# Performance work log

Hardware: AMD Instinct MI355X
Metric: run time of the kernel (lower is better)

The kernel has to match this reference:

```python
import jax, jax.numpy as jnp
import numpy as np

# Per-layer (in_dim, hidden) for the 6 stacked LSTM layers:
# rnn_inp: (1,64),(64,64),(64,64); rnn_out: (64,1),(1,1),(1,1)
_LAYER_DIMS = [(1, 64), (64, 64), (64, 64), (64, 1), (1, 1), (1, 1)]
_LAYER_NAMES = ['a0', 'a1', 'a2', 'b0', 'b1', 'b2']


def _lstm_layer(x, w_ih, w_hh, b_ih, b_hh):
    """Single unidirectional LSTM layer, PyTorch gate order (i, f, g, o).
    x: [B, T, Din]; w_ih: [4H, Din]; w_hh: [4H, H]; biases: [4H]. Returns [B, T, H]."""
    H = w_hh.shape[1]
    B = x.shape[0]
    # Input projection for all timesteps at once (one big GEMM).
    pre = jnp.einsum('btd,gd->btg', x, w_ih) + b_ih + b_hh  # [B, T, 4H]
    pre_t = jnp.swapaxes(pre, 0, 1)  # [T, B, 4H]

    def step(carry, xt):
        h, c = carry
        gates = xt + h @ w_hh.T  # [B, 4H]
        i, f, g, o = jnp.split(gates, 4, axis=-1)
        i = jax.nn.sigmoid(i)
        f = jax.nn.sigmoid(f)
        g = jnp.tanh(g)
        o = jax.nn.sigmoid(o)
        c = f * c + i * g
        h = o * jnp.tanh(c)
        return (h, c), h

    h0 = jnp.zeros((B, H), x.dtype)
    (_, _), hs = jax.lax.scan(step, (h0, h0), pre_t)  # hs: [T, B, H]
    return jnp.swapaxes(hs, 0, 1)


def setup_inputs() -> dict:
    key = jax.random.key(0)
    B, T = 256, 512
    inp = {}
    k, key = jax.random.split(key)
    inp['x'] = jax.random.normal(k, (B, T, 1), dtype=jnp.float32)
    for name, (din, h) in zip(_LAYER_NAMES, _LAYER_DIMS):
        s = 1.0 / np.sqrt(h)  # PyTorch LSTM init scale U(-1/sqrt(H), 1/sqrt(H))
        k1, k2, k3, k4, key = jax.random.split(key, 5)
        inp[f'w_ih_{name}'] = jax.random.uniform(k1, (4 * h, din), jnp.float32, -s, s)
        inp[f'w_hh_{name}'] = jax.random.uniform(k2, (4 * h, h), jnp.float32, -s, s)
        inp[f'b_ih_{name}'] = jax.random.uniform(k3, (4 * h,), jnp.float32, -s, s)
        inp[f'b_hh_{name}'] = jax.random.uniform(k4, (4 * h,), jnp.float32, -s, s)
    return inp


def reference(x,
              w_ih_a0, w_hh_a0, b_ih_a0, b_hh_a0,
              w_ih_a1, w_hh_a1, b_ih_a1, b_hh_a1,
              w_ih_a2, w_hh_a2, b_ih_a2, b_hh_a2,
              w_ih_b0, w_hh_b0, b_ih_b0, b_hh_b0,
              w_ih_b1, w_hh_b1, b_ih_b1, b_hh_b1,
              w_ih_b2, w_hh_b2, b_ih_b2, b_hh_b2):
    layers = [
        (w_ih_a0, w_hh_a0, b_ih_a0, b_hh_a0),
        (w_ih_a1, w_hh_a1, b_ih_a1, b_hh_a1),
        (w_ih_a2, w_hh_a2, b_ih_a2, b_hh_a2),
        (w_ih_b0, w_hh_b0, b_ih_b0, b_hh_b0),
        (w_ih_b1, w_hh_b1, b_ih_b1, b_hh_b1),
        (w_ih_b2, w_hh_b2, b_ih_b2, b_hh_b2),
    ]
    h = x
    for w_ih, w_hh, b_ih, b_hh in layers:
        h = _lstm_layer(h, w_ih, w_hh, b_ih, b_hh)
    # activation between the two LSTM stacks is identity (activation_type='identity')
    return h  # [B, T, 1]
```

## Files before the change

kernel.cpp:

```cpp
#include <hip/hip_runtime.h>


#define BB 256
#define TT 512
#define CH 4
#define NS 8

typedef _Float16 v2h __attribute__((ext_vector_type(2)));

__device__ __forceinline__ float sig_(float x) {
  return __builtin_amdgcn_rcpf(1.f + __builtin_amdgcn_exp2f(-1.44269504f * x));
}
__device__ __forceinline__ float tanh_(float x) {
  return __builtin_fmaf(2.f, __builtin_amdgcn_rcpf(1.f + __builtin_amdgcn_exp2f(-2.88539008f * x)), -1.f);
}

template <int K>
__device__ __forceinline__ float qb_(float v) {
  return __int_as_float(__builtin_amdgcn_update_dpp(
      0, __float_as_int(v), (K | (K << 2) | (K << 4) | (K << 6)), 0xF, 0xF, true));
}

__device__ __forceinline__ void ldsbar_() {
  asm volatile("s_waitcnt lgkmcnt(0)\n\ts_barrier" ::: "memory");
}

#if __has_builtin(__builtin_amdgcn_fdot2)
#define FDOT2(acc, a, b) (acc) = __builtin_amdgcn_fdot2((a), (b), (acc), false)
#else
#define FDOT2(acc, a, b) \
  (acc) = __builtin_fmaf((float)(a)[0], (float)(b)[0], \
          __builtin_fmaf((float)(a)[1], (float)(b)[1], (acc)))
#endif
#define KEEPP(a) asm volatile("" : "+v"(a))
#define PIN32(w)                                                            \
  do {                                                                      \
    _Pragma("unroll") for (int _i = 0; _i < 32; ++_i) KEEPP((w)[_i]);       \
  } while (0)

__device__ __forceinline__ v2h bc2h_(int v) { return __builtin_bit_cast(v2h, v); }

__device__ __forceinline__ void load_h64(const _Float16* p, v2h hv[32]) {
  const int4* hp = reinterpret_cast<const int4*>(p);
#pragma unroll
  for (int i = 0; i < 8; ++i) {
    int4 blk = hp[i];
    hv[4 * i + 0] = bc2h_(blk.x);
    hv[4 * i + 1] = bc2h_(blk.y);
    hv[4 * i + 2] = bc2h_(blk.z);
    hv[4 * i + 3] = bc2h_(blk.w);
  }
}

__device__ __forceinline__ void load_row16(const float* src, v2h dst[32]) {
  const float4* p = reinterpret_cast<const float4*>(src);
#pragma unroll
  for (int i = 0; i < 16; ++i) {
    float4 v = p[i];
    dst[2 * i]     = v2h{(_Float16)v.x, (_Float16)v.y};
    dst[2 * i + 1] = v2h{(_Float16)v.z, (_Float16)v.w};
  }
}

__device__ __forceinline__ void dot4_(const v2h w[4][32], const v2h hv[32],
                                      float& p0, float& p1, float& p2, float& p3) {
  float a0 = p0, a1 = p1, a2 = p2, a3 = p3;
  float b0 = 0.f, b1 = 0.f, b2 = 0.f, b3 = 0.f;
#pragma unroll
  for (int j = 0; j < 32; j += 2) {
    FDOT2(a0, w[0][j], hv[j]);         FDOT2(a1, w[1][j], hv[j]);
    FDOT2(a2, w[2][j], hv[j]);         FDOT2(a3, w[3][j], hv[j]);
    FDOT2(b0, w[0][j + 1], hv[j + 1]); FDOT2(b1, w[1][j + 1], hv[j + 1]);
    FDOT2(b2, w[2][j + 1], hv[j + 1]); FDOT2(b3, w[3][j + 1], hv[j + 1]);
  }
  p0 = a0 + b0; p1 = a1 + b1; p2 = a2 + b2; p3 = a3 + b3;
}

__device__ __forceinline__ void dot2g_(const v2h* w0, const v2h* w1,
                                       const v2h hv[32], float& p0, float& p1) {
  float a0 = 0.f, a1 = 0.f, b0 = 0.f, b1 = 0.f;
#pragma unroll
  for (int j = 0; j < 32; j += 2) {
    FDOT2(a0, w0[j], hv[j]);         FDOT2(a1, w1[j], hv[j]);
    FDOT2(b0, w0[j + 1], hv[j + 1]); FDOT2(b1, w1[j + 1], hv[j + 1]);
  }
  p0 = a0 + b0; p1 = a1 + b1;
}

__global__ __attribute__((amdgpu_flat_work_group_size(512, 512),
                          amdgpu_waves_per_eu(1, 2)))
void lstm_pipe_k(
    const float* __restrict__ x,
    const float* __restrict__ wih_a0, const float* __restrict__ whh_a0,
    const float* __restrict__ bih_a0, const float* __restrict__ bhh_a0,
    const float* __restrict__ wih_a1, const float* __restrict__ whh_a1,
    const float* __restrict__ bih_a1, const float* __restrict__ bhh_a1,
    const float* __restrict__ wih_a2, const float* __restrict__ whh_a2,
    const float* __restrict__ bih_a2, const float* __restrict__ bhh_a2,
    const float* __restrict__ wih_b0, const float* __restrict__ whh_b0,
    const float* __restrict__ bih_b0, const float* __restrict__ bhh_b0,
    const float* __restrict__ wih_b1, const float* __restrict__ whh_b1,
    const float* __restrict__ bih_b1, const float* __restrict__ bhh_b1,
    const float* __restrict__ wih_b2, const float* __restrict__ whh_b2,
    const float* __restrict__ bih_b2, const float* __restrict__ bhh_b2,
    float* __restrict__ out)
{
  asm volatile("" ::: "v190", "v191");

  const int b = blockIdx.x;
  const int tid = threadIdx.x;
  const int wave = tid >> 6;
  const int lane = tid & 63;

  __shared__ __align__(16) _Float16 hh[3][NS][64];
  __shared__ __align__(16) float pj[2][NS][256];
  __shared__ float xs[TT];

  for (int i = tid; i < TT; i += 512) xs[i] = x[(size_t)b * TT + i];
  for (int i = tid; i < 3 * NS * 64 / 2; i += 512) reinterpret_cast<int*>(hh)[i] = 0;

  v2h wt[4][32];
  float bias[4] = {0.f, 0.f, 0.f, 0.f};
  float wi0_[4] = {0.f, 0.f, 0.f, 0.f};
  float whb0[4] = {}, wi1b[4] = {}, wh1b[4] = {}, bb1[4] = {},
        wi2b[4] = {}, wh2b[4] = {}, bb2[4] = {};

  if (wave == 0) {
#pragma unroll
    for (int q = 0; q < 4; ++q) {
      const int row = q * 64 + lane;
      load_row16(whh_a0 + row * 64, wt[q]);
      bias[q] = bih_a0[row] + bhh_a0[row];
      wi0_[q] = wih_a0[row];
    }
    PIN32(wt[0]); PIN32(wt[1]); PIN32(wt[2]); PIN32(wt[3]);
  } else if (wave == 1) {
#pragma unroll
    for (int q = 0; q < 4; ++q) {
      const int row = q * 64 + lane;
      load_row16(whh_a1 + row * 64, wt[q]);
      bias[q] = bih_a1[row] + bhh_a1[row];
    }
    PIN32(wt[0]); PIN32(wt[1]); PIN32(wt[2]); PIN32(wt[3]);
  } else if (wave == 2) {
#pragma unroll
    for (int q = 0; q < 4; ++q) {
      const int row = q * 64 + lane;
      load_row16(whh_a2 + row * 64, wt[q]);
      bias[q] = bih_a2[row] + bhh_a2[row];
    }
    PIN32(wt[0]); PIN32(wt[1]); PIN32(wt[2]); PIN32(wt[3]);
  } else if (wave == 3) {
    const int q = lane & 3;
    load_row16(wih_b0 + q * 64, wt[0]);
    bias[0] = bih_b0[q] + bhh_b0[q];
#pragma unroll
    for (int k = 0; k < 4; ++k) {
      whb0[k] = whh_b0[k];
      wi1b[k] = wih_b1[k]; wh1b[k] = whh_b1[k]; bb1[k] = bih_b1[k] + bhh_b1[k];
      wi2b[k] = wih_b2[k]; wh2b[k] = whh_b2[k]; bb2[k] = bih_b2[k] + bhh_b2[k];
    }
    PIN32(wt[0]);
  } else if (wave == 4) {
#pragma unroll
    for (int q = 0; q < 2; ++q) load_row16(wih_a1 + (q * 64 + lane) * 64, wt[q]);
    PIN32(wt[0]); PIN32(wt[1]);
  } else if (wave == 5) {
#pragma unroll
    for (int q = 0; q < 2; ++q) load_row16(wih_a1 + ((q + 2) * 64 + lane) * 64, wt[q]);
    PIN32(wt[0]); PIN32(wt[1]);
  } else if (wave == 6) {
#pragma unroll
    for (int q = 0; q < 2; ++q) load_row16(wih_a2 + (q * 64 + lane) * 64, wt[q]);
    PIN32(wt[0]); PIN32(wt[1]);
  } else {
#pragma unroll
    for (int q = 0; q < 2; ++q) load_row16(wih_a2 + ((q + 2) * 64 + lane) * 64, wt[q]);
    PIN32(wt[0]); PIN32(wt[1]);
  }
  __syncthreads();

  float c = 0.f;
  float h0b = 0.f, c0b = 0.f, h1b = 0.f, c1b = 0.f, h2b = 0.f, c2b = 0.f;

  const int NE = TT / CH + 5;
  for (int e = 0; e < NE; ++e) {
    if (wave == 0) {
      const int t0 = e * CH;
      if (t0 < TT) {
        __builtin_amdgcn_s_setprio(1);
        for (int s = 0; s < CH; ++s) {
          const int t = t0 + s;
          v2h hv[32];
          load_h64(&hh[0][(t + NS - 1) & (NS - 1)][0], hv);
          const float xv = xs[t];
          float p0 = bias[0], p1 = bias[1], p2 = bias[2], p3 = bias[3];
          dot4_(wt, hv, p0, p1, p2, p3);
          p0 = __builtin_fmaf(wi0_[0], xv, p0);
          p1 = __builtin_fmaf(wi0_[1], xv, p1);
          p2 = __builtin_fmaf(wi0_[2], xv, p2);
          p3 = __builtin_fmaf(wi0_[3], xv, p3);
          float gi = sig_(p0), gf = sig_(p1), gg = tanh_(p2), go = sig_(p3);
          c = __builtin_fmaf(gf, c, gi * gg);
          hh[0][t & (NS - 1)][lane] = (_Float16)(go * tanh_(c));
          asm volatile("s_waitcnt lgkmcnt(0)" ::: "memory");
        }
        __builtin_amdgcn_s_setprio(0);
      }
    } else if (wave == 1) {
      const int t0 = (e - 2) * CH;
      if (t0 >= 0 && t0 < TT) {
        __builtin_amdgcn_s_setprio(1);
        for (int s = 0; s < CH; ++s) {
          const int t = t0 + s;
          v2h hv[32];
          load_h64(&hh[1][(t + NS - 1) & (NS - 1)][0], hv);
          float4 pr = *reinterpret_cast<const float4*>(&pj[0][t & (NS - 1)][lane * 4]);
          float p0 = bias[0], p1 = bias[1], p2 = bias[2], p3 = bias[3];
          dot4_(wt, hv, p0, p1, p2, p3);
          p0 += pr.x; p1 += pr.y; p2 += pr.z; p3 += pr.w;
          float gi = sig_(p0), gf = sig_(p1), gg = tanh_(p2), go = sig_(p3);
          c = __builtin_fmaf(gf, c, gi * gg);
          hh[1][t & (NS - 1)][lane] = (_Float16)(go * tanh_(c));
          asm volatile("s_waitcnt lgkmcnt(0)" ::: "memory");
        }
        __builtin_amdgcn_s_setprio(0);
      }
    } else if (wave == 2) {
      const int t0 = (e - 4) * CH;
      if (t0 >= 0 && t0 < TT) {
        __builtin_amdgcn_s_setprio(1);
        for (int s = 0; s < CH; ++s) {
          const int t = t0 + s;
          v2h hv[32];
          load_h64(&hh[2][(t + NS - 1) & (NS - 1)][0], hv);
          float4 pr = *reinterpret_cast<const float4*>(&pj[1][t & (NS - 1)][lane * 4]);
          float p0 = bias[0], p1 = bias[1], p2 = bias[2], p3 = bias[3];
          dot4_(wt, hv, p0, p1, p2, p3);
          p0 += pr.x; p1 += pr.y; p2 += pr.z; p3 += pr.w;
          float gi = sig_(p0), gf = sig_(p1), gg = tanh_(p2), go = sig_(p3);
          c = __builtin_fmaf(gf, c, gi * gg);
          hh[2][t & (NS - 1)][lane] = (_Float16)(go * tanh_(c));
          asm volatile("s_waitcnt lgkmcnt(0)" ::: "memory");
        }
        __builtin_amdgcn_s_setprio(0);
      }
    } else if (wave == 3) {
      const int t0 = (e - 5) * CH;
      if (t0 >= 0 && t0 < TT) {
        for (int s = 0; s < CH; ++s) {
          const int t = t0 + s;
          v2h hv[32];
          load_h64(&hh[2][t & (NS - 1)][0], hv);
          float pga = bias[0], pgb = 0.f;
#pragma unroll
          for (int j = 0; j < 32; j += 2) {
            FDOT2(pga, wt[0][j], hv[j]);
            FDOT2(pgb, wt[0][j + 1], hv[j + 1]);
          }
          float pg = pga + pgb;
          float p_i = qb_<0>(pg), p_f = qb_<1>(pg), p_g = qb_<2>(pg), p_o = qb_<3>(pg);
          float i0 = sig_(__builtin_fmaf(whb0[0], h0b, p_i));
          float f0 = sig_(__builtin_fmaf(whb0[1], h0b, p_f));
          float g0 = tanh_(__builtin_fmaf(whb0[2], h0b, p_g));
          float o0 = sig_(__builtin_fmaf(whb0[3], h0b, p_o));
          c0b = __builtin_fmaf(f0, c0b, i0 * g0);
          h0b = o0 * tanh_(c0b);
          float i1 = sig_(bb1[0] + __builtin_fmaf(wi1b[0], h0b, wh1b[0] * h1b));
          float f1 = sig_(bb1[1] + __builtin_fmaf(wi1b[1], h0b, wh1b[1] * h1b));
          float g1 = tanh_(bb1[2] + __builtin_fmaf(wi1b[2], h0b, wh1b[2] * h1b));
          float o1 = sig_(bb1[3] + __builtin_fmaf(wi1b[3], h0b, wh1b[3] * h1b));
          c1b = __builtin_fmaf(f1, c1b, i1 * g1);
          h1b = o1 * tanh_(c1b);
          float i2 = sig_(bb2[0] + __builtin_fmaf(wi2b[0], h1b, wh2b[0] * h2b));
          float f2 = sig_(bb2[1] + __builtin_fmaf(wi2b[1], h1b, wh2b[1] * h2b));
          float g2 = tanh_(bb2[2] + __builtin_fmaf(wi2b[2], h1b, wh2b[2] * h2b));
          float o2 = sig_(bb2[3] + __builtin_fmaf(wi2b[3], h1b, wh2b[3] * h2b));
          c2b = __builtin_fmaf(f2, c2b, i2 * g2);
          h2b = o2 * tanh_(c2b);
          if (lane == 0) out[(size_t)b * TT + t] = h2b;
        }
      }
    } else if (wave == 4) {
      const int t0 = (e - 1) * CH;
      if (t0 >= 0 && t0 < TT) {
        for (int s = 0; s < CH; ++s) {
          const int t = t0 + s;
          v2h hv[32];
          load_h64(&hh[0][t & (NS - 1)][0], hv);
          float p0, p1;
          dot2g_(wt[0], wt[1], hv, p0, p1);
          *reinterpret_cast<float2*>(&pj[0][t & (NS - 1)][lane * 4]) = float2{p0, p1};
        }
      }
    } else if (wave == 5) {
      const int t0 = (e - 1) * CH;
      if (t0 >= 0 && t0 < TT) {
        for (int s = 0; s < CH; ++s) {
          const int t = t0 + s;
          v2h hv[32];
          load_h64(&hh[0][t & (NS - 1)][0], hv);
          float p2, p3;
          dot2g_(wt[0], wt[1], hv, p2, p3);
          *reinterpret_cast<float2*>(&pj[0][t & (NS - 1)][lane * 4 + 2]) = float2{p2, p3};
        }
      }
    } else if (wave == 6) {
      const int t0 = (e - 3) * CH;
      if (t0 >= 0 && t0 < TT) {
        for (int s = 0; s < CH; ++s) {
          const int t = t0 + s;
          v2h hv[32];
          load_h64(&hh[1][t & (NS - 1)][0], hv);
          float p0, p1;
          dot2g_(wt[0], wt[1], hv, p0, p1);
          *reinterpret_cast<float2*>(&pj[1][t & (NS - 1)][lane * 4]) = float2{p0, p1};
        }
      }
    } else {
      const int t0 = (e - 3) * CH;
      if (t0 >= 0 && t0 < TT) {
        for (int s = 0; s < CH; ++s) {
          const int t = t0 + s;
          v2h hv[32];
          load_h64(&hh[1][t & (NS - 1)][0], hv);
          float p2, p3;
          dot2g_(wt[0], wt[1], hv, p2, p3);
          *reinterpret_cast<float2*>(&pj[1][t & (NS - 1)][lane * 4 + 2]) = float2{p2, p3};
        }
      }
    }
    ldsbar_();
  }
}

extern "C" void kernel_launch(void* const* d_in, const int* in_sizes, int n_in,
                              void* d_out, int out_size, void* d_ws, size_t ws_size,
                              hipStream_t stream) {
  const float* x      = (const float*)d_in[0];
  const float* wih_a0 = (const float*)d_in[1];
  const float* whh_a0 = (const float*)d_in[2];
  const float* bih_a0 = (const float*)d_in[3];
  const float* bhh_a0 = (const float*)d_in[4];
  const float* wih_a1 = (const float*)d_in[5];
  const float* whh_a1 = (const float*)d_in[6];
  const float* bih_a1 = (const float*)d_in[7];
  const float* bhh_a1 = (const float*)d_in[8];
  const float* wih_a2 = (const float*)d_in[9];
  const float* whh_a2 = (const float*)d_in[10];
  const float* bih_a2 = (const float*)d_in[11];
  const float* bhh_a2 = (const float*)d_in[12];
  const float* wih_b0 = (const float*)d_in[13];
  const float* whh_b0 = (const float*)d_in[14];
  const float* bih_b0 = (const float*)d_in[15];
  const float* bhh_b0 = (const float*)d_in[16];
  const float* wih_b1 = (const float*)d_in[17];
  const float* whh_b1 = (const float*)d_in[18];
  const float* bih_b1 = (const float*)d_in[19];
  const float* bhh_b1 = (const float*)d_in[20];
  const float* wih_b2 = (const float*)d_in[21];
  const float* whh_b2 = (const float*)d_in[22];
  const float* bih_b2 = (const float*)d_in[23];
  const float* bhh_b2 = (const float*)d_in[24];
  float* out = (float*)d_out;

  lstm_pipe_k<<<BB, 512, 0, stream>>>(
      x,
      wih_a0, whh_a0, bih_a0, bhh_a0,
      wih_a1, whh_a1, bih_a1, bhh_a1,
      wih_a2, whh_a2, bih_a2, bhh_a2,
      wih_b0, whh_b0, bih_b0, bhh_b0,
      wih_b1, whh_b1, bih_b1, bhh_b1,
      wih_b2, whh_b2, bih_b2, bhh_b2,
      out);
}
```

Before: 401.5 us.

## Spill half of recurrent weights to LDS to fit two blocks per CU

Each recurrent wave now keeps only the first 32 columns of its 256x64 W_hh slice in registers and stages the rest as packed fp16 rows in LDS. Each step reads those rows back with int4 loads. This halves weight register pressure, so waves_per_eu can rise to 2 and two 512-thread blocks can share a CU. It also doubles the pipeline chunk (CH 8, NS 16) to halve barrier count, and drops the per-step lgkmcnt waits after the h stores. The cost is extra LDS traffic on the serial recurrence critical path and more shared memory per block. Removing the explicit waits may weaken ordering of the h writes within a chunk.

```diff
diff --git a/kernel.cpp b/kernel.cpp
--- a/kernel.cpp
+++ b/kernel.cpp
@@ -3,8 +3,8 @@
 
 #define BB 256
 #define TT 512
-#define CH 4
-#define NS 8
+#define CH 8
+#define NS 16
 
 typedef _Float16 v2h __attribute__((ext_vector_type(2)));
 
@@ -33,12 +33,15 @@
           __builtin_fmaf((float)(a)[1], (float)(b)[1], (acc)))
 #endif
 #define KEEPP(a) asm volatile("" : "+v"(a))
-#define PIN32(w)                                                            \
+#define PIN16(w)                                                            \
   do {                                                                      \
-    _Pragma("unroll") for (int _i = 0; _i < 32; ++_i) KEEPP((w)[_i]);       \
+    _Pragma("unroll") for (int _i = 0; _i < 16; ++_i) KEEPP((w)[_i]);       \
   } while (0)
 
 __device__ __forceinline__ v2h bc2h_(int v) { return __builtin_bit_cast(v2h, v); }
+__device__ __forceinline__ int pk2_(float x, float y) {
+  return __builtin_bit_cast(int, v2h{(_Float16)x, (_Float16)y});
+}
 
 __device__ __forceinline__ void load_h64(const _Float16* p, v2h hv[32]) {
   const int4* hp = reinterpret_cast<const int4*>(p);
@@ -52,43 +55,95 @@
   }
 }
 
-__device__ __forceinline__ void load_row16(const float* src, v2h dst[32]) {
+__device__ __forceinline__ void load_row_pair(const float* src, v2h lo[16], v2h hi[16]) {
   const float4* p = reinterpret_cast<const float4*>(src);
 #pragma unroll
-  for (int i = 0; i < 16; ++i) {
+  for (int i = 0; i < 8; ++i) {
     float4 v = p[i];
-    dst[2 * i]     = v2h{(_Float16)v.x, (_Float16)v.y};
-    dst[2 * i + 1] = v2h{(_Float16)v.z, (_Float16)v.w};
-  }
-}
-
-__device__ __forceinline__ void dot4_(const v2h w[4][32], const v2h hv[32],
-                                      float& p0, float& p1, float& p2, float& p3) {
+    lo[2 * i]     = v2h{(_Float16)v.x, (_Float16)v.y};
+    lo[2 * i + 1] = v2h{(_Float16)v.z, (_Float16)v.w};
+  }
+#pragma unroll
+  for (int i = 0; i < 8; ++i) {
+    float4 v = p[8 + i];
+    hi[2 * i]     = v2h{(_Float16)v.x, (_Float16)v.y};
+    hi[2 * i + 1] = v2h{(_Float16)v.z, (_Float16)v.w};
+  }
+}
+
+__device__ __forceinline__ void load_rec_w(const float* W, int lane,
+                                           v2h wt[4][16], unsigned char* wl) {
+#pragma unroll
+  for (int q = 0; q < 4; ++q) {
+    const int row = q * 64 + lane;
+    const float4* p = reinterpret_cast<const float4*>(W + row * 64);
+#pragma unroll
+    for (int i = 0; i < 8; ++i) {
+      float4 v = p[i];
+      wt[q][2 * i]     = v2h{(_Float16)v.x, (_Float16)v.y};
+      wt[q][2 * i + 1] = v2h{(_Float16)v.z, (_Float16)v.w};
+    }
+#pragma unroll
+    for (int i = 0; i < 4; ++i) {
+      float4 va = p[8 + 2 * i], vb = p[9 + 2 * i];
+      int4 blk;
+      blk.x = pk2_(va.x, va.y); blk.y = pk2_(va.z, va.w);
+      blk.z = pk2_(vb.x, vb.y); blk.w = pk2_(vb.z, vb.w);
+      *reinterpret_cast<int4*>(wl + row * 80 + i * 16) = blk;
+    }
+  }
+}
+
+__device__ __forceinline__ void dot4full_(const v2h wt[4][16],
+                                          const unsigned char* wl, int lane,
+                                          const v2h hv[32],
+                                          float& p0, float& p1, float& p2, float& p3) {
   float a0 = p0, a1 = p1, a2 = p2, a3 = p3;
   float b0 = 0.f, b1 = 0.f, b2 = 0.f, b3 = 0.f;
 #pragma unroll
-  for (int j = 0; j < 32; j += 2) {
-    FDOT2(a0, w[0][j], hv[j]);         FDOT2(a1, w[1][j], hv[j]);
-    FDOT2(a2, w[2][j], hv[j]);         FDOT2(a3, w[3][j], hv[j]);
-    FDOT2(b0, w[0][j + 1], hv[j + 1]); FDOT2(b1, w[1][j + 1], hv[j + 1]);
-    FDOT2(b2, w[2][j + 1], hv[j + 1]); FDOT2(b3, w[3][j + 1], hv[j + 1]);
+  for (int j = 0; j < 16; j += 2) {
+    FDOT2(a0, wt[0][j], hv[j]);         FDOT2(a1, wt[1][j], hv[j]);
+    FDOT2(a2, wt[2][j], hv[j]);         FDOT2(a3, wt[3][j], hv[j]);
+    FDOT2(b0, wt[0][j + 1], hv[j + 1]); FDOT2(b1, wt[1][j + 1], hv[j + 1]);
+    FDOT2(b2, wt[2][j + 1], hv[j + 1]); FDOT2(b3, wt[3][j + 1], hv[j + 1]);
+  }
+  const int rb0 = lane * 80, rb1 = (64 + lane) * 80,
+            rb2 = (128 + lane) * 80, rb3 = (192 + lane) * 80;
+#pragma unroll
+  for (int jb = 0; jb < 4; ++jb) {
+    int4 w0 = *reinterpret_cast<const int4*>(wl + rb0 + jb * 16);
+    int4 w1 = *reinterpret_cast<const int4*>(wl + rb1 + jb * 16);
+    int4 w2 = *reinterpret_cast<const int4*>(wl + rb2 + jb * 16);
+    int4 w3 = *reinterpret_cast<const int4*>(wl + rb3 + jb * 16);
+    const int h0 = 16 + jb * 4;
+    FDOT2(a0, bc2h_(w0.x), hv[h0 + 0]); FDOT2(b0, bc2h_(w0.y), hv[h0 + 1]);
+    FDOT2(a0, bc2h_(w0.z), hv[h0 + 2]); FDOT2(b0, bc2h_(w0.w), hv[h0 + 3]);
+    FDOT2(a1, bc2h_(w1.x), hv[h0 + 0]); FDOT2(b1, bc2h_(w1.y), hv[h0 + 1]);
+    FDOT2(a1, bc2h_(w1.z), hv[h0 + 2]); FDOT2(b1, bc2h_(w1.w), hv[h0 + 3]);
+    FDOT2(a2, bc2h_(w2.x), hv[h0 + 0]); FDOT2(b2, bc2h_(w2.y), hv[h0 + 1]);
+    FDOT2(a2, bc2h_(w2.z), hv[h0 + 2]); FDOT2(b2, bc2h_(w2.w), hv[h0 + 3]);
+    FDOT2(a3, bc2h_(w3.x), hv[h0 + 0]); FDOT2(b3, bc2h_(w3.y), hv[h0 + 1]);
+    FDOT2(a3, bc2h_(w3.z), hv[h0 + 2]); FDOT2(b3, bc2h_(w3.w), hv[h0 + 3]);
   }
   p0 = a0 + b0; p1 = a1 + b1; p2 = a2 + b2; p3 = a3 + b3;
 }
 
-__device__ __forceinline__ void dot2g_(const v2h* w0, const v2h* w1,
+__device__ __forceinline__ void dot2g_(const v2h* wa_lo, const v2h* wa_hi,
+                                       const v2h* wb_lo, const v2h* wb_hi,
                                        const v2h hv[32], float& p0, float& p1) {
   float a0 = 0.f, a1 = 0.f, b0 = 0.f, b1 = 0.f;
 #pragma unroll
-  for (int j = 0; j < 32; j += 2) {
-    FDOT2(a0, w0[j], hv[j]);         FDOT2(a1, w1[j], hv[j]);
-    FDOT2(b0, w0[j + 1], hv[j + 1]); FDOT2(b1, w1[j + 1], hv[j + 1]);
+  for (int j = 0; j < 16; j += 2) {
+    FDOT2(a0, wa_lo[j], hv[j]);          FDOT2(b0, wa_lo[j + 1], hv[j + 1]);
+    FDOT2(a0, wa_hi[j], hv[16 + j]);     FDOT2(b0, wa_hi[j + 1], hv[17 + j]);
+    FDOT2(a1, wb_lo[j], hv[j]);          FDOT2(b1, wb_lo[j + 1], hv[j + 1]);
+    FDOT2(a1, wb_hi[j], hv[16 + j]);     FDOT2(b1, wb_hi[j + 1], hv[17 + j]);
   }
   p0 = a0 + b0; p1 = a1 + b1;
 }
 
 __global__ __attribute__((amdgpu_flat_work_group_size(512, 512),
-                          amdgpu_waves_per_eu(1, 2)))
+                          amdgpu_waves_per_eu(2, 2)))
 void lstm_pipe_k(
     const float* __restrict__ x,
     const float* __restrict__ wih_a0, const float* __restrict__ whh_a0,
@@ -105,8 +160,6 @@
     const float* __restrict__ bih_b2, const float* __restrict__ bhh_b2,
     float* __restrict__ out)
 {
-  asm volatile("" ::: "v190", "v191");
-
   const int b = blockIdx.x;
   const int tid = threadIdx.x;
   const int wave = tid >> 6;
@@ -114,45 +167,46 @@
 
   __shared__ __align__(16) _Float16 hh[3][NS][64];
   __shared__ __align__(16) float pj[2][NS][256];
+  __shared__ __align__(16) unsigned char wlds[3][256 * 80];
   __shared__ float xs[TT];
 
   for (int i = tid; i < TT; i += 512) xs[i] = x[(size_t)b * TT + i];
   for (int i = tid; i < 3 * NS * 64 / 2; i += 512) reinterpret_cast<int*>(hh)[i] = 0;
 
-  v2h wt[4][32];
+  v2h wt[4][16];
   float bias[4] = {0.f, 0.f, 0.f, 0.f};
   float wi0_[4] = {0.f, 0.f, 0.f, 0.f};
   float whb0[4] = {}, wi1b[4] = {}, wh1b[4] = {}, bb1[4] = {},
         wi2b[4] = {}, wh2b[4] = {}, bb2[4] = {};
 
   if (wave == 0) {
+    load_rec_w(whh_a0, lane, wt, &wlds[0][0]);
 #pragma unroll
     for (int q = 0; q < 4; ++q) {
       const int row = q * 64 + lane;
-      load_row16(whh_a0 + row * 64, wt[q]);
       bias[q] = bih_a0[row] + bhh_a0[row];
       wi0_[q] = wih_a0[row];
     }
-    PIN32(wt[0]); PIN32(wt[1]); PIN32(wt[2]); PIN32(wt[3]);
+    PIN16(wt[0]); PIN16(wt[1]); PIN16(wt[2]); PIN16(wt[3]);
   } else if (wave == 1) {
+    load_rec_w(whh_a1, lane, wt, &wlds[1][0]);
 #pragma unroll
     for (int q = 0; q < 4; ++q) {
       const int row = q * 64 + lane;
-      load_row16(whh_a1 + row * 64, wt[q]);
       bias[q] = bih_a1[row] + bhh_a1[row];
     }
-    PIN32(wt[0]); PIN32(wt[1]); PIN32(wt[2]); PIN32(wt[3]);
+    PIN16(wt[0]); PIN16(wt[1]); PIN16(wt[2]); PIN16(wt[3]);
   } else if (wave == 2) {
+    load_rec_w(whh_a2, lane, wt, &wlds[2][0]);
 #pragma unroll
     for (int q = 0; q < 4; ++q) {
       const int row = q * 64 + lane;
-      load_row16(whh_a2 + row * 64, wt[q]);
       bias[q] = bih_a2[row] + bhh_a2[row];
     }
-    PIN32(wt[0]); PIN32(wt[1]); PIN32(wt[2]); PIN32(wt[3]);
+    PIN16(wt[0]); PIN16(wt[1]); PIN16(wt[2]); PIN16(wt[3]);
   } else if (wave == 3) {
     const int q = lane & 3;
-    load_row16(wih_b0 + q * 64, wt[0]);
+    load_row_pair(wih_b0 + q * 64, wt[0], wt[1]);
     bias[0] = bih_b0[q] + bhh_b0[q];
 #pragma unroll
     for (int k = 0; k < 4; ++k) {
@@ -160,23 +214,23 @@
       wi1b[k] = wih_b1[k]; wh1b[k] = whh_b1[k]; bb1[k] = bih_b1[k] + bhh_b1[k];
       wi2b[k] = wih_b2[k]; wh2b[k] = whh_b2[k]; bb2[k] = bih_b2[k] + bhh_b2[k];
     }
-    PIN32(wt[0]);
+    PIN16(wt[0]); PIN16(wt[1]);
   } else if (wave == 4) {
-#pragma unroll
-    for (int q = 0; q < 2; ++q) load_row16(wih_a1 + (q * 64 + lane) * 64, wt[q]);
-    PIN32(wt[0]); PIN32(wt[1]);
+    load_row_pair(wih_a1 + (0 * 64 + lane) * 64, wt[0], wt[1]);
+    load_row_pair(wih_a1 + (1 * 64 + lane) * 64, wt[2], wt[3]);
+    PIN16(wt[0]); PIN16(wt[1]); PIN16(wt[2]); PIN16(wt[3]);
   } else if (wave == 5) {
-#pragma unroll
-    for (int q = 0; q < 2; ++q) load_row16(wih_a1 + ((q + 2) * 64 + lane) * 64, wt[q]);
-    PIN32(wt[0]); PIN32(wt[1]);
+    load_row_pair(wih_a1 + (2 * 64 + lane) * 64, wt[0], wt[1]);
+    load_row_pair(wih_a1 + (3 * 64 + lane) * 64, wt[2], wt[3]);
+    PIN16(wt[0]); PIN16(wt[1]); PIN16(wt[2]); PIN16(wt[3]);
   } else if (wave == 6) {
-#pragma unroll
-    for (int q = 0; q < 2; ++q) load_row16(wih_a2 + (q * 64 + lane) * 64, wt[q]);
-    PIN32(wt[0]); PIN32(wt[1]);
+    load_row_pair(wih_a2 + (0 * 64 + lane) * 64, wt[0], wt[1]);
+    load_row_pair(wih_a2 + (1 * 64 + lane) * 64, wt[2], wt[3]);
+    PIN16(wt[0]); PIN16(wt[1]); PIN16(wt[2]); PIN16(wt[3]);
   } else {
-#pragma unroll
-    for (int q = 0; q < 2; ++q) load_row16(wih_a2 + ((q + 2) * 64 + lane) * 64, wt[q]);
-    PIN32(wt[0]); PIN32(wt[1]);
+    load_row_pair(wih_a2 + (2 * 64 + lane) * 64, wt[0], wt[1]);
+    load_row_pair(wih_a2 + (3 * 64 + lane) * 64, wt[2], wt[3]);
+    PIN16(wt[0]); PIN16(wt[1]); PIN16(wt[2]); PIN16(wt[3]);
   }
   __syncthreads();
 
@@ -195,7 +249,7 @@
           load_h64(&hh[0][(t + NS - 1) & (NS - 1)][0], hv);
           const float xv = xs[t];
           float p0 = bias[0], p1 = bias[1], p2 = bias[2], p3 = bias[3];
-          dot4_(wt, hv, p0, p1, p2, p3);
+          dot4full_(wt, &wlds[0][0], lane, hv, p0, p1, p2, p3);
           p0 = __builtin_fmaf(wi0_[0], xv, p0);
           p1 = __builtin_fmaf(wi0_[1], xv, p1);
           p2 = __builtin_fmaf(wi0_[2], xv, p2);
@@ -203,7 +257,6 @@
           float gi = sig_(p0), gf = sig_(p1), gg = tanh_(p2), go = sig_(p3);
           c = __builtin_fmaf(gf, c, gi * gg);
           hh[0][t & (NS - 1)][lane] = (_Float16)(go * tanh_(c));
-          asm volatile("s_waitcnt lgkmcnt(0)" ::: "memory");
         }
         __builtin_amdgcn_s_setprio(0);
       }
@@ -217,12 +270,11 @@
           load_h64(&hh[1][(t + NS - 1) & (NS - 1)][0], hv);
           float4 pr = *reinterpret_cast<const float4*>(&pj[0][t & (NS - 1)][lane * 4]);
           float p0 = bias[0], p1 = bias[1], p2 = bias[2], p3 = bias[3];
-          dot4_(wt, hv, p0, p1, p2, p3);
+          dot4full_(wt, &wlds[1][0], lane, hv, p0, p1, p2, p3);
           p0 += pr.x; p1 += pr.y; p2 += pr.z; p3 += pr.w;
           float gi = sig_(p0), gf = sig_(p1), gg = tanh_(p2), go = sig_(p3);
           c = __builtin_fmaf(gf, c, gi * gg);
           hh[1][t & (NS - 1)][lane] = (_Float16)(go * tanh_(c));
-          asm volatile("s_waitcnt lgkmcnt(0)" ::: "memory");
         }
         __builtin_amdgcn_s_setprio(0);
       }
@@ -236,12 +288,11 @@
           load_h64(&hh[2][(t + NS - 1) & (NS - 1)][0], hv);
           float4 pr = *reinterpret_cast<const float4*>(&pj[1][t & (NS - 1)][lane * 4]);
           float p0 = bias[0], p1 = bias[1], p2 = bias[2], p3 = bias[3];
-          dot4_(wt, hv, p0, p1, p2, p3);
+          dot4full_(wt, &wlds[2][0], lane, hv, p0, p1, p2, p3);
           p0 += pr.x; p1 += pr.y; p2 += pr.z; p3 += pr.w;
           float gi = sig_(p0), gf = sig_(p1), gg = tanh_(p2), go = sig_(p3);
           c = __builtin_fmaf(gf, c, gi * gg);
           hh[2][t & (NS - 1)][lane] = (_Float16)(go * tanh_(c));
-          asm volatile("s_waitcnt lgkmcnt(0)" ::: "memory");
         }
         __builtin_amdgcn_s_setprio(0);
       }
@@ -254,9 +305,9 @@
           load_h64(&hh[2][t & (NS - 1)][0], hv);
           float pga = bias[0], pgb = 0.f;
 #pragma unroll
-          for (int j = 0; j < 32; j += 2) {
+          for (int j = 0; j < 16; ++j) {
             FDOT2(pga, wt[0][j], hv[j]);
-            FDOT2(pgb, wt[0][j + 1], hv[j + 1]);
+            FDOT2(pgb, wt[1][j], hv[16 + j]);
           }
           float pg = pga + pgb;
           float p_i = qb_<0>(pg), p_f = qb_<1>(pg), p_g = qb_<2>(pg), p_o = qb_<3>(pg);
@@ -289,7 +340,7 @@
           v2h hv[32];
           load_h64(&hh[0][t & (NS - 1)][0], hv);
           float p0, p1;
-          dot2g_(wt[0], wt[1], hv, p0, p1);
+          dot2g_(wt[0], wt[1], wt[2], wt[3], hv, p0, p1);
           *reinterpret_cast<float2*>(&pj[0][t & (NS - 1)][lane * 4]) = float2{p0, p1};
         }
       }
@@ -301,7 +352,7 @@
           v2h hv[32];
           load_h64(&hh[0][t & (NS - 1)][0], hv);
           float p2, p3;
-          dot2g_(wt[0], wt[1], hv, p2, p3);
+          dot2g_(wt[0], wt[1], wt[2], wt[3], hv, p2, p3);
           *reinterpret_cast<float2*>(&pj[0][t & (NS - 1)][lane * 4 + 2]) = float2{p2, p3};
         }
       }
@@ -313,7 +364,7 @@
           v2h hv[32];
           load_h64(&hh[1][t & (NS - 1)][0], hv);
           float p0, p1;
-          dot2g_(wt[0], wt[1], hv, p0, p1);
+          dot2g_(wt[0], wt[1], wt[2], wt[3], hv, p0, p1);
           *reinterpret_cast<float2*>(&pj[1][t & (NS - 1)][lane * 4]) = float2{p0, p1};
         }
       }
@@ -325,7 +376,7 @@
           v2h hv[32];
           load_h64(&hh[1][t & (NS - 1)][0], hv);
           float p2, p3;
-          dot2g_(wt[0], wt[1], hv, p2, p3);
+          dot2g_(wt[0], wt[1], wt[2], wt[3], hv, p2, p3);
           *reinterpret_cast<float2*>(&pj[1][t & (NS - 1)][lane * 4 + 2]) = float2{p2, p3};
         }
       }
```

Measured after the change: 410.4 us. 2.2% more time.

## Replace lockstep barriers with per-wave LDS progress flags and MFMA input projections

Applied to the files above, without the earlier changes.

The per-epoch block-wide barrier pipeline is replaced by producer/consumer progress counters in LDS. Each wave spins on an acquire-load of its upstream stage's counter and publishes its own with a release-store. The four FDOT2-based input-projection waves are collapsed into two waves that compute the 64x256 projection for a chunk of 8 timesteps with 16x16x32 f16 MFMA. Chunk size and ring depth are doubled, and the block shrinks to 384 threads. This aims to stop fast stages from waiting on the slowest wave every epoch and to cut projection work. The cost is spin-wait overhead, more registers for the MFMA fragments, and correctness risk in the slot-reuse dependencies.

```diff
diff --git a/kernel.cpp b/kernel.cpp
--- a/kernel.cpp
+++ b/kernel.cpp
@@ -3,10 +3,13 @@
 
 #define BB 256
 #define TT 512
-#define CH 4
-#define NS 8
+#define CH 8
+#define NS 16
+#define NW (TT / CH)
 
 typedef _Float16 v2h __attribute__((ext_vector_type(2)));
+typedef _Float16 v8h __attribute__((ext_vector_type(8)));
+typedef float v4f __attribute__((ext_vector_type(4)));
 
 __device__ __forceinline__ float sig_(float x) {
   return __builtin_amdgcn_rcpf(1.f + __builtin_amdgcn_exp2f(-1.44269504f * x));
@@ -19,10 +22,6 @@
 __device__ __forceinline__ float qb_(float v) {
   return __int_as_float(__builtin_amdgcn_update_dpp(
       0, __float_as_int(v), (K | (K << 2) | (K << 4) | (K << 6)), 0xF, 0xF, true));
-}
-
-__device__ __forceinline__ void ldsbar_() {
-  asm volatile("s_waitcnt lgkmcnt(0)\n\ts_barrier" ::: "memory");
 }
 
 #if __has_builtin(__builtin_amdgcn_fdot2)
@@ -37,6 +36,23 @@
   do {                                                                      \
     _Pragma("unroll") for (int _i = 0; _i < 32; ++_i) KEEPP((w)[_i]);       \
   } while (0)
+#define PIN16(w)                                                            \
+  do {                                                                      \
+    _Pragma("unroll") for (int _i = 0; _i < 16; ++_i) KEEPP((w)[_i]);       \
+  } while (0)
+
+#define WAITP(i, v)                                                           \
+  while (__hip_atomic_load(&prog[i], __ATOMIC_ACQUIRE,                        \
+                           __HIP_MEMORY_SCOPE_WORKGROUP) < (v)) {             \
+    __builtin_amdgcn_s_sleep(1);                                              \
+  }
+#define POSTP(i, v)                                                           \
+  do {                                                                        \
+    asm volatile("s_waitcnt lgkmcnt(0)" ::: "memory");                        \
+    if (lane == 0)                                                            \
+      __hip_atomic_store(&prog[i], (v), __ATOMIC_RELEASE,                     \
+                         __HIP_MEMORY_SCOPE_WORKGROUP);                       \
+  } while (0)
 
 __device__ __forceinline__ v2h bc2h_(int v) { return __builtin_bit_cast(v2h, v); }
 
@@ -62,6 +78,31 @@
   }
 }
 
+__device__ __forceinline__ void load_row_pair(const float* src, v2h* lo, v2h* hi) {
+  const float4* p = reinterpret_cast<const float4*>(src);
+#pragma unroll
+  for (int i = 0; i < 8; ++i) {
+    float4 v = p[i];
+    lo[2 * i]     = v2h{(_Float16)v.x, (_Float16)v.y};
+    lo[2 * i + 1] = v2h{(_Float16)v.z, (_Float16)v.w};
+  }
+#pragma unroll
+  for (int i = 0; i < 8; ++i) {
+    float4 v = p[8 + i];
+    hi[2 * i]     = v2h{(_Float16)v.x, (_Float16)v.y};
+    hi[2 * i + 1] = v2h{(_Float16)v.z, (_Float16)v.w};
+  }
+}
+
+__device__ __forceinline__ v8h ldbfrag_(const float* W, int t, int kc, int lane) {
+  const int row = 16 * t + (lane & 15);
+  const float* p = W + row * 64 + 32 * kc + 4 * (lane >> 4);
+  float4 fa = *reinterpret_cast<const float4*>(p);
+  float4 fb = *reinterpret_cast<const float4*>(p + 16);
+  return v8h{(_Float16)fa.x, (_Float16)fa.y, (_Float16)fa.z, (_Float16)fa.w,
+             (_Float16)fb.x, (_Float16)fb.y, (_Float16)fb.z, (_Float16)fb.w};
+}
+
 __device__ __forceinline__ void dot4_(const v2h w[4][32], const v2h hv[32],
                                       float& p0, float& p1, float& p2, float& p3) {
   float a0 = p0, a1 = p1, a2 = p2, a3 = p3;
@@ -76,19 +117,8 @@
   p0 = a0 + b0; p1 = a1 + b1; p2 = a2 + b2; p3 = a3 + b3;
 }
 
-__device__ __forceinline__ void dot2g_(const v2h* w0, const v2h* w1,
-                                       const v2h hv[32], float& p0, float& p1) {
-  float a0 = 0.f, a1 = 0.f, b0 = 0.f, b1 = 0.f;
-#pragma unroll
-  for (int j = 0; j < 32; j += 2) {
-    FDOT2(a0, w0[j], hv[j]);         FDOT2(a1, w1[j], hv[j]);
-    FDOT2(b0, w0[j + 1], hv[j + 1]); FDOT2(b1, w1[j + 1], hv[j + 1]);
-  }
-  p0 = a0 + b0; p1 = a1 + b1;
-}
-
-__global__ __attribute__((amdgpu_flat_work_group_size(512, 512),
-                          amdgpu_waves_per_eu(1, 2)))
+__global__ __attribute__((amdgpu_flat_work_group_size(384, 384),
+                          amdgpu_waves_per_eu(2, 2)))
 void lstm_pipe_k(
     const float* __restrict__ x,
     const float* __restrict__ wih_a0, const float* __restrict__ whh_a0,
@@ -105,8 +135,6 @@
     const float* __restrict__ bih_b2, const float* __restrict__ bhh_b2,
     float* __restrict__ out)
 {
-  asm volatile("" ::: "v190", "v191");
-
   const int b = blockIdx.x;
   const int tid = threadIdx.x;
   const int wave = tid >> 6;
@@ -115,11 +143,14 @@
   __shared__ __align__(16) _Float16 hh[3][NS][64];
   __shared__ __align__(16) float pj[2][NS][256];
   __shared__ float xs[TT];
-
-  for (int i = tid; i < TT; i += 512) xs[i] = x[(size_t)b * TT + i];
-  for (int i = tid; i < 3 * NS * 64 / 2; i += 512) reinterpret_cast<int*>(hh)[i] = 0;
+  __shared__ int prog[6];
+
+  for (int i = tid; i < TT; i += 384) xs[i] = x[(size_t)b * TT + i];
+  for (int i = tid; i < 3 * NS * 64 / 2; i += 384) reinterpret_cast<int*>(hh)[i] = 0;
+  if (tid < 6) prog[tid] = 0;
 
   v2h wt[4][32];
+  v8h bfr[16][2];
   float bias[4] = {0.f, 0.f, 0.f, 0.f};
   float wi0_[4] = {0.f, 0.f, 0.f, 0.f};
   float whb0[4] = {}, wi1b[4] = {}, wh1b[4] = {}, bb1[4] = {},
@@ -152,7 +183,7 @@
     PIN32(wt[0]); PIN32(wt[1]); PIN32(wt[2]); PIN32(wt[3]);
   } else if (wave == 3) {
     const int q = lane & 3;
-    load_row16(wih_b0 + q * 64, wt[0]);
+    load_row_pair(wih_b0 + q * 64, wt[0], wt[1]);
     bias[0] = bih_b0[q] + bhh_b0[q];
 #pragma unroll
     for (int k = 0; k < 4; ++k) {
@@ -160,177 +191,186 @@
       wi1b[k] = wih_b1[k]; wh1b[k] = whh_b1[k]; bb1[k] = bih_b1[k] + bhh_b1[k];
       wi2b[k] = wih_b2[k]; wh2b[k] = whh_b2[k]; bb2[k] = bih_b2[k] + bhh_b2[k];
     }
-    PIN32(wt[0]);
+    PIN16(wt[0]); PIN16(wt[1]);
   } else if (wave == 4) {
 #pragma unroll
-    for (int q = 0; q < 2; ++q) load_row16(wih_a1 + (q * 64 + lane) * 64, wt[q]);
-    PIN32(wt[0]); PIN32(wt[1]);
-  } else if (wave == 5) {
-#pragma unroll
-    for (int q = 0; q < 2; ++q) load_row16(wih_a1 + ((q + 2) * 64 + lane) * 64, wt[q]);
-    PIN32(wt[0]); PIN32(wt[1]);
-  } else if (wave == 6) {
-#pragma unroll
-    for (int q = 0; q < 2; ++q) load_row16(wih_a2 + (q * 64 + lane) * 64, wt[q]);
-    PIN32(wt[0]); PIN32(wt[1]);
+    for (int t = 0; t < 16; ++t) {
+      bfr[t][0] = ldbfrag_(wih_a1, t, 0, lane);
+      bfr[t][1] = ldbfrag_(wih_a1, t, 1, lane);
+    }
   } else {
 #pragma unroll
-    for (int q = 0; q < 2; ++q) load_row16(wih_a2 + ((q + 2) * 64 + lane) * 64, wt[q]);
-    PIN32(wt[0]); PIN32(wt[1]);
+    for (int t = 0; t < 16; ++t) {
+      bfr[t][0] = ldbfrag_(wih_a2, t, 0, lane);
+      bfr[t][1] = ldbfrag_(wih_a2, t, 1, lane);
+    }
   }
   __syncthreads();
 
   float c = 0.f;
   float h0b = 0.f, c0b = 0.f, h1b = 0.f, c1b = 0.f, h2b = 0.f, c2b = 0.f;
 
-  const int NE = TT / CH + 5;
-  for (int e = 0; e < NE; ++e) {
-    if (wave == 0) {
-      const int t0 = e * CH;
-      if (t0 < TT) {
-        __builtin_amdgcn_s_setprio(1);
-        for (int s = 0; s < CH; ++s) {
-          const int t = t0 + s;
-          v2h hv[32];
-          load_h64(&hh[0][(t + NS - 1) & (NS - 1)][0], hv);
-          const float xv = xs[t];
-          float p0 = bias[0], p1 = bias[1], p2 = bias[2], p3 = bias[3];
-          dot4_(wt, hv, p0, p1, p2, p3);
-          p0 = __builtin_fmaf(wi0_[0], xv, p0);
-          p1 = __builtin_fmaf(wi0_[1], xv, p1);
-          p2 = __builtin_fmaf(wi0_[2], xv, p2);
-          p3 = __builtin_fmaf(wi0_[3], xv, p3);
-          float gi = sig_(p0), gf = sig_(p1), gg = tanh_(p2), go = sig_(p3);
-          c = __builtin_fmaf(gf, c, gi * gg);
-          hh[0][t & (NS - 1)][lane] = (_Float16)(go * tanh_(c));
-          asm volatile("s_waitcnt lgkmcnt(0)" ::: "memory");
+  if (wave == 0) {
+    __builtin_amdgcn_s_setprio(1);
+    for (int k = 0; k < NW; ++k) {
+      if (k >= 2) { WAITP(4, k - 1); }
+      const int t0 = k * CH;
+      for (int s = 0; s < CH; ++s) {
+        const int t = t0 + s;
+        v2h hv[32];
+        load_h64(&hh[0][(t + NS - 1) & (NS - 1)][0], hv);
+        const float xv = xs[t];
+        float p0 = bias[0], p1 = bias[1], p2 = bias[2], p3 = bias[3];
+        dot4_(wt, hv, p0, p1, p2, p3);
+        p0 = __builtin_fmaf(wi0_[0], xv, p0);
+        p1 = __builtin_fmaf(wi0_[1], xv, p1);
+        p2 = __builtin_fmaf(wi0_[2], xv, p2);
+        p3 = __builtin_fmaf(wi0_[3], xv, p3);
+        float gi = sig_(p0), gf = sig_(p1), gg = tanh_(p2), go = sig_(p3);
+        c = __builtin_fmaf(gf, c, gi * gg);
+        hh[0][t & (NS - 1)][lane] = (_Float16)(go * tanh_(c));
+      }
+      POSTP(0, k + 1);
+    }
+    __builtin_amdgcn_s_setprio(0);
+  } else if (wave == 1) {
+    __builtin_amdgcn_s_setprio(1);
+    for (int k = 0; k < NW; ++k) {
+      WAITP(4, k + 1);
+      if (k >= 2) { WAITP(5, k - 1); }
+      const int t0 = k * CH;
+      for (int s = 0; s < CH; ++s) {
+        const int t = t0 + s;
+        v2h hv[32];
+        load_h64(&hh[1][(t + NS - 1) & (NS - 1)][0], hv);
+        float4 pr = *reinterpret_cast<const float4*>(&pj[0][t & (NS - 1)][lane * 4]);
+        float p0 = bias[0], p1 = bias[1], p2 = bias[2], p3 = bias[3];
+        dot4_(wt, hv, p0, p1, p2, p3);
+        p0 += pr.x; p1 += pr.y; p2 += pr.z; p3 += pr.w;
+        float gi = sig_(p0), gf = sig_(p1), gg = tanh_(p2), go = sig_(p3);
+        c = __builtin_fmaf(gf, c, gi * gg);
+        hh[1][t & (NS - 1)][lane] = (_Float16)(go * tanh_(c));
+      }
+      POSTP(1, k + 1);
+    }
+    __builtin_amdgcn_s_setprio(0);
+  } else if (wave == 2) {
+    __builtin_amdgcn_s_setprio(1);
+    for (int k = 0; k < NW; ++k) {
+      WAITP(5, k + 1);
+      if (k >= 2) { WAITP(3, k - 1); }
+      const int t0 = k * CH;
+      for (int s = 0; s < CH; ++s) {
+        const int t = t0 + s;
+        v2h hv[32];
+        load_h64(&hh[2][(t + NS - 1) & (NS - 1)][0], hv);
+        float4 pr = *reinterpret_cast<const float4*>(&pj[1][t & (NS - 1)][lane * 4]);
+        float p0 = bias[0], p1 = bias[1], p2 = bias[2], p3 = bias[3];
+        dot4_(wt, hv, p0, p1, p2, p3);
+        p0 += pr.x; p1 += pr.y; p2 += pr.z; p3 += pr.w;
+        float gi = sig_(p0), gf = sig_(p1), gg = tanh_(p2), go = sig_(p3);
+        c = __builtin_fmaf(gf, c, gi * gg);
+        hh[2][t & (NS - 1)][lane] = (_Float16)(go * tanh_(c));
+      }
+      POSTP(2, k + 1);
+    }
+    __builtin_amdgcn_s_setprio(0);
+  } else if (wave == 3) {
+    for (int k = 0; k < NW; ++k) {
+      WAITP(2, k + 1);
+      const int t0 = k * CH;
+      for (int s = 0; s < CH; ++s) {
+        const int t = t0 + s;
+        v2h hv[32];
+        load_h64(&hh[2][t & (NS - 1)][0], hv);
+        float pga = bias[0], pgb = 0.f;
+#pragma unroll
+        for (int j = 0; j < 16; ++j) {
+          FDOT2(pga, wt[0][j], hv[j]);
+          FDOT2(pgb, wt[1][j], hv[16 + j]);
         }
-        __builtin_amdgcn_s_setprio(0);
-      }
-    } else if (wave == 1) {
-      const int t0 = (e - 2) * CH;
-      if (t0 >= 0 && t0 < TT) {
-        __builtin_amdgcn_s_setprio(1);
-        for (int s = 0; s < CH; ++s) {
-          const int t = t0 + s;
-          v2h hv[32];
-          load_h64(&hh[1][(t + NS - 1) & (NS - 1)][0], hv);
-          float4 pr = *reinterpret_cast<const float4*>(&pj[0][t & (NS - 1)][lane * 4]);
-          float p0 = bias[0], p1 = bias[1], p2 = bias[2], p3 = bias[3];
-          dot4_(wt, hv, p0, p1, p2, p3);
-          p0 += pr.x; p1 += pr.y; p2 += pr.z; p3 += pr.w;
-          float gi = sig_(p0), gf = sig_(p1), gg = tanh_(p2), go = sig_(p3);
-          c = __builtin_fmaf(gf, c, gi * gg);
-          hh[1][t & (NS - 1)][lane] = (_Float16)(go * tanh_(c));
-          asm volatile("s_waitcnt lgkmcnt(0)" ::: "memory");
+        float pg = pga + pgb;
+        float p_i = qb_<0>(pg), p_f = qb_<1>(pg), p_g = qb_<2>(pg), p_o = qb_<3>(pg);
+        float i0 = sig_(__builtin_fmaf(whb0[0], h0b, p_i));
+        float f0 = sig_(__builtin_fmaf(whb0[1], h0b, p_f));
+        float g0 = tanh_(__builtin_fmaf(whb0[2], h0b, p_g));
+        float o0 = sig_(__builtin_fmaf(whb0[3], h0b, p_o));
+        c0b = __builtin_fmaf(f0, c0b, i0 * g0);
+        h0b = o0 * tanh_(c0b);
+        float i1 = sig_(bb1[0] + __builtin_fmaf(wi1b[0], h0b, wh1b[0] * h1b));
+        float f1 = sig_(bb1[1] + __builtin_fmaf(wi1b[1], h0b, wh1b[1] * h1b));
+        float g1 = tanh_(bb1[2] + __builtin_fmaf(wi1b[2], h0b, wh1b[2] * h1b));
+        float o1 = sig_(bb1[3] + __builtin_fmaf(wi1b[3], h0b, wh1b[3] * h1b));
+        c1b = __builtin_fmaf(f1, c1b, i1 * g1);
+        h1b = o1 * tanh_(c1b);
+        float i2 = sig_(bb2[0] + __builtin_fmaf(wi2b[0], h1b, wh2b[0] * h2b));
+        float f2 = sig_(bb2[1] + __builtin_fmaf(wi2b[1], h1b, wh2b[1] * h2b));
+        float g2 = tanh_(bb2[2] + __builtin_fmaf(wi2b[2], h1b, wh2b[2] * h2b));
+        float o2 = sig_(bb2[3] + __builtin_fmaf(wi2b[3], h1b, wh2b[3] * h2b));
+        c2b = __builtin_fmaf(f2, c2b, i2 * g2);
+        h2b = o2 * tanh_(c2b);
+        if (lane == 0) out[(size_t)b * TT + t] = h2b;
+      }
+      POSTP(3, k + 1);
+    }
+  } else if (wave == 4) {
+    for (int k = 0; k < NW; ++k) {
+      WAITP(0, k + 1);
+      if (k >= 2) { WAITP(1, k - 1); }
+      const int t0 = k * CH;
+      const int slotb = (t0 + (lane & 15)) & (NS - 1);
+      const char* hp = (const char*)(&hh[0][slotb][0]) + 8 * (lane >> 4);
+      int2 r00 = *(const int2*)(hp);
+      int2 r01 = *(const int2*)(hp + 32);
+      int2 r10 = *(const int2*)(hp + 64);
+      int2 r11 = *(const int2*)(hp + 96);
+      v8h Bf0 = __builtin_bit_cast(v8h, int4{r00.x, r00.y, r01.x, r01.y});
+      v8h Bf1 = __builtin_bit_cast(v8h, int4{r10.x, r10.y, r11.x, r11.y});
+      float* pbase = &pj[0][slotb][0] + 16 * (lane >> 4);
+      const bool wr = (lane & 15) < 8;
+      const v4f z = {0.f, 0.f, 0.f, 0.f};
+#pragma unroll
+      for (int tl = 0; tl < 16; ++tl) {
+        v4f acc = __builtin_amdgcn_mfma_f32_16x16x32_f16(bfr[tl][0], Bf0, z, 0, 0, 0);
+        acc = __builtin_amdgcn_mfma_f32_16x16x32_f16(bfr[tl][1], Bf1, acc, 0, 0, 0);
+        if (wr) {
+          const int o = 64 * (tl & 3) + (tl >> 2);
+          pbase[o] = acc[0]; pbase[o + 4] = acc[1];
+          pbase[o + 8] = acc[2]; pbase[o + 12] = acc[3];
         }
-        __builtin_amdgcn_s_setprio(0);
-      }
-    } else if (wave == 2) {
-      const int t0 = (e - 4) * CH;
-      if (t0 >= 0 && t0 < TT) {
-        __builtin_amdgcn_s_setprio(1);
-        for (int s = 0; s < CH; ++s) {
-          const int t = t0 + s;
-          v2h hv[32];
-          load_h64(&hh[2][(t + NS - 1) & (NS - 1)][0], hv);
-          float4 pr = *reinterpret_cast<const float4*>(&pj[1][t & (NS - 1)][lane * 4]);
-          float p0 = bias[0], p1 = bias[1], p2 = bias[2], p3 = bias[3];
-          dot4_(wt, hv, p0, p1, p2, p3);
-          p0 += pr.x; p1 += pr.y; p2 += pr.z; p3 += pr.w;
-          float gi = sig_(p0), gf = sig_(p1), gg = tanh_(p2), go = sig_(p3);
-          c = __builtin_fmaf(gf, c, gi * gg);
-          hh[2][t & (NS - 1)][lane] = (_Float16)(go * tanh_(c));
-          asm volatile("s_waitcnt lgkmcnt(0)" ::: "memory");
+        __builtin_amdgcn_sched_barrier(0);
+      }
+      POSTP(4, k + 1);
+    }
+  } else {
+    for (int k = 0; k < NW; ++k) {
+      WAITP(1, k + 1);
+      if (k >= 2) { WAITP(2, k - 1); }
+      const int t0 = k * CH;
+      const int slotb = (t0 + (lane & 15)) & (NS - 1);
+      const char* hp = (const char*)(&hh[1][slotb][0]) + 8 * (lane >> 4);
+      int2 r00 = *(const int2*)(hp);
+      int2 r01 = *(const int2*)(hp + 32);
+      int2 r10 = *(const int2*)(hp + 64);
+      int2 r11 = *(const int2*)(hp + 96);
+      v8h Bf0 = __builtin_bit_cast(v8h, int4{r00.x, r00.y, r01.x, r01.y});
+      v8h Bf1 = __builtin_bit_cast(v8h, int4{r10.x, r10.y, r11.x, r11.y});
+      float* pbase = &pj[1][slotb][0] + 16 * (lane >> 4);
+      const bool wr = (lane & 15) < 8;
+      const v4f z = {0.f, 0.f, 0.f, 0.f};
+#pragma unroll
+      for (int tl = 0; tl < 16; ++tl) {
+        v4f acc = __builtin_amdgcn_mfma_f32_16x16x32_f16(bfr[tl][0], Bf0, z, 0, 0, 0);
+        acc = __builtin_amdgcn_mfma_f32_16x16x32_f16(bfr[tl][1], Bf1, acc, 0, 0, 0);
+        if (wr) {
+          const int o = 64 * (tl & 3) + (tl >> 2);
+          pbase[o] = acc[0]; pbase[o + 4] = acc[1];
+          pbase[o + 8] = acc[2]; pbase[o + 12] = acc[3];
         }
-        __builtin_amdgcn_s_setprio(0);
-      }
-    } else if (wave == 3) {
-      const int t0 = (e - 5) * CH;
-      if (t0 >= 0 && t0 < TT) {
-        for (int s = 0; s < CH; ++s) {
-          const int t = t0 + s;
-          v2h hv[32];
-          load_h64(&hh[2][t & (NS - 1)][0], hv);
-          float pga = bias[0], pgb = 0.f;
-#pragma unroll
-          for (int j = 0; j < 32; j += 2) {
-            FDOT2(pga, wt[0][j], hv[j]);
-            FDOT2(pgb, wt[0][j + 1], hv[j + 1]);
-          }
-          float pg = pga + pgb;
-          float p_i = qb_<0>(pg), p_f = qb_<1>(pg), p_g = qb_<2>(pg), p_o = qb_<3>(pg);
-          float i0 = sig_(__builtin_fmaf(whb0[0], h0b, p_i));
-          float f0 = sig_(__builtin_fmaf(whb0[1], h0b, p_f));
-          float g0 = tanh_(__builtin_fmaf(whb0[2], h0b, p_g));
-          float o0 = sig_(__builtin_fmaf(whb0[3], h0b, p_o));
-          c0b = __builtin_fmaf(f0, c0b, i0 * g0);
-          h0b = o0 * tanh_(c0b);
-          float i1 = sig_(bb1[0] + __builtin_fmaf(wi1b[0], h0b, wh1b[0] * h1b));
-          float f1 = sig_(bb1[1] + __builtin_fmaf(wi1b[1], h0b, wh1b[1] * h1b));
-          float g1 = tanh_(bb1[2] + __builtin_fmaf(wi1b[2], h0b, wh1b[2] * h1b));
-          float o1 = sig_(bb1[3] + __builtin_fmaf(wi1b[3], h0b, wh1b[3] * h1b));
-          c1b = __builtin_fmaf(f1, c1b, i1 * g1);
-          h1b = o1 * tanh_(c1b);
-          float i2 = sig_(bb2[0] + __builtin_fmaf(wi2b[0], h1b, wh2b[0] * h2b));
-          float f2 = sig_(bb2[1] + __builtin_fmaf(wi2b[1], h1b, wh2b[1] * h2b));
-          float g2 = tanh_(bb2[2] + __builtin_fmaf(wi2b[2], h1b, wh2b[2] * h2b));
-          float o2 = sig_(bb2[3] + __builtin_fmaf(wi2b[3], h1b, wh2b[3] * h2b));
-          c2b = __builtin_fmaf(f2, c2b, i2 * g2);
-          h2b = o2 * tanh_(c2b);
-          if (lane == 0) out[(size_t)b * TT + t] = h2b;
-        }
-      }
-    } else if (wave == 4) {
-      const int t0 = (e - 1) * CH;
-      if (t0 >= 0 && t0 < TT) {
-        for (int s = 0; s < CH; ++s) {
-          const int t = t0 + s;
-          v2h hv[32];
-          load_h64(&hh[0][t & (NS - 1)][0], hv);
-          float p0, p1;
-          dot2g_(wt[0], wt[1], hv, p0, p1);
-          *reinterpret_cast<float2*>(&pj[0][t & (NS - 1)][lane * 4]) = float2{p0, p1};
-        }
-      }
-    } else if (wave == 5) {
-      const int t0 = (e - 1) * CH;
-      if (t0 >= 0 && t0 < TT) {
-        for (int s = 0; s < CH; ++s) {
-          const int t = t0 + s;
-          v2h hv[32];
-          load_h64(&hh[0][t & (NS - 1)][0], hv);
-          float p2, p3;
-          dot2g_(wt[0], wt[1], hv, p2, p3);
-          *reinterpret_cast<float2*>(&pj[0][t & (NS - 1)][lane * 4 + 2]) = float2{p2, p3};
-        }
-      }
-    } else if (wave == 6) {
-      const int t0 = (e - 3) * CH;
-      if (t0 >= 0 && t0 < TT) {
-        for (int s = 0; s < CH; ++s) {
-          const int t = t0 + s;
-          v2h hv[32];
-          load_h64(&hh[1][t & (NS - 1)][0], hv);
-          float p0, p1;
-          dot2g_(wt[0], wt[1], hv, p0, p1);
-          *reinterpret_cast<float2*>(&pj[1][t & (NS - 1)][lane * 4]) = float2{p0, p1};
-        }
-      }
-    } else {
-      const int t0 = (e - 3) * CH;
-      if (t0 >= 0 && t0 < TT) {
-        for (int s = 0; s < CH; ++s) {
-          const int t = t0 + s;
-          v2h hv[32];
-          load_h64(&hh[1][t & (NS - 1)][0], hv);
-          float p2, p3;
-          dot2g_(wt[0], wt[1], hv, p2, p3);
-          *reinterpret_cast<float2*>(&pj[1][t & (NS - 1)][lane * 4 + 2]) = float2{p2, p3};
-        }
-      }
-    }
-    ldsbar_();
+        __builtin_amdgcn_sched_barrier(0);
+      }
+      POSTP(5, k + 1);
+    }
   }
 }
 
@@ -364,7 +404,7 @@
   const float* bhh_b2 = (const float*)d_in[24];
   float* out = (float*)d_out;
 
-  lstm_pipe_k<<<BB, 512, 0, stream>>>(
+  lstm_pipe_k<<<BB, 384, 0, stream>>>(
       x,
       wih_a0, whh_a0, bih_a0, bhh_a0,
       wih_a1, whh_a1, bih_a1, bhh_a1,
```

Measured after the change: 389.1 us. 1.03x faster.
